# Optimization experiments

Hardware: AMD Instinct MI355X
Metric: run time of the kernel (lower is better)

The kernel has to match this reference:

```python
import jax, jax.numpy as jnp
import numpy as np

N_NODES = 100000
N_EDGES = 1600000


def _tconv(x, src, dst, Wq, bq, Wk, bk, Wv, bv, Ws, bs):
    """PyG TransformerConv (heads=1, concat=True, root_weight=True), eval mode."""
    n = x.shape[0]
    q = x @ Wq + bq          # [N, d]
    k = x @ Wk + bk
    v = x @ Wv + bv
    scale = 1.0 / jnp.sqrt(jnp.asarray(q.shape[1], q.dtype))
    # per-edge attention logits: query at destination, key at source
    alpha = jnp.sum(q[dst] * k[src], axis=-1) * scale       # [E]
    # segment softmax over incoming edges of each destination node
    m = jax.ops.segment_max(alpha, dst, num_segments=n)      # [N]
    e = jnp.exp(alpha - m[dst])
    s = jax.ops.segment_sum(e, dst, num_segments=n)          # [N]
    a = e / s[dst]                                           # [E]
    agg = jax.ops.segment_sum(a[:, None] * v[src], dst, num_segments=n)  # [N, d]
    return agg + x @ Ws + bs  # skip connection (root_weight=True)


def setup_inputs() -> dict:
    key = jax.random.key(0)
    ks = jax.random.split(key, 20)
    x = jax.random.normal(ks[0], (N_NODES, 2), dtype=jnp.float32)
    edge_index = jax.random.randint(ks[1], (2, N_EDGES), 0, N_NODES, dtype=jnp.int64)
    def lin(k, din, dout):
        k1, k2 = jax.random.split(k)
        lim = 1.0 / np.sqrt(din)
        W = jax.random.uniform(k1, (din, dout), jnp.float32, -lim, lim)
        b = jax.random.uniform(k2, (dout,), jnp.float32, -lim, lim)
        return W, b
    Wq1, bq1 = lin(ks[2], 2, 256)
    Wk1, bk1 = lin(ks[3], 2, 256)
    Wv1, bv1 = lin(ks[4], 2, 256)
    Ws1, bs1 = lin(ks[5], 2, 256)
    Wq2, bq2 = lin(ks[6], 256, 2)
    Wk2, bk2 = lin(ks[7], 256, 2)
    Wv2, bv2 = lin(ks[8], 256, 2)
    Ws2, bs2 = lin(ks[9], 256, 2)
    return dict(x=x, edge_index=edge_index,
                Wq1=Wq1, bq1=bq1, Wk1=Wk1, bk1=bk1, Wv1=Wv1, bv1=bv1, Ws1=Ws1, bs1=bs1,
                Wq2=Wq2, bq2=bq2, Wk2=Wk2, bk2=bk2, Wv2=Wv2, bv2=bv2, Ws2=Ws2, bs2=bs2)


def reference(x, edge_index,
              Wq1, bq1, Wk1, bk1, Wv1, bv1, Ws1, bs1,
              Wq2, bq2, Wk2, bk2, Wv2, bv2, Ws2, bs2):
    src, dst = edge_index[0], edge_index[1]
    h = _tconv(x, src, dst, Wq1, bq1, Wk1, bk1, Wv1, bv1, Ws1, bs1)
    h = jax.nn.relu(h)
    # F.dropout is identity in eval mode
    h = _tconv(h, src, dst, Wq2, bq2, Wk2, bk2, Wv2, bv2, Ws2, bs2)
    return jax.nn.log_softmax(h, axis=1)
```

## Files before the change

kernel.cpp:

```cpp
#include <hip/hip_runtime.h>


#define R_LOG2   8
#define R_DSTS   256
#define BE       4096
#define MAXNB    512
#define S_SLICES 8
#define RSQRT2   0.70710678118654752f

__device__ __forceinline__ int wave_excl_scan(int v, int lane, int& total) {
    int incl = v;
#pragma unroll
    for (int o = 1; o < 64; o <<= 1) {
        int t = __shfl_up(incl, o);
        if (lane >= o) incl += t;
    }
    total = __shfl(incl, 63);
    return incl - v;
}

__global__ void coeff_k(const float* __restrict__ Wq1, const float* __restrict__ bq1,
                        const float* __restrict__ Wk1, const float* __restrict__ bk1,
                        float* __restrict__ coeff) {
    __shared__ float part[4][9];
    int c = threadIdx.x;
    float wq0 = Wq1[c], wq1 = Wq1[256 + c];
    float wk0 = Wk1[c], wk1 = Wk1[256 + c];
    float bq = bq1[c], bk = bk1[c];
    float vals[9] = { wq0 * wk0, wq0 * wk1, wq1 * wk0, wq1 * wk1,
                      wq0 * bk,  wq1 * bk,  bq * wk0,  bq * wk1,  bq * bk };
    int lane = c & 63, w = c >> 6;
#pragma unroll
    for (int i = 0; i < 9; ++i) {
        float v = vals[i];
#pragma unroll
        for (int o = 32; o > 0; o >>= 1) v += __shfl_xor(v, o);
        if (lane == 0) part[w][i] = v;
    }
    __syncthreads();
    if (c < 9) coeff[c] = part[0][c] + part[1][c] + part[2][c] + part[3][c];
}

__global__ __launch_bounds__(256) void count_k(
        const int* __restrict__ dst, int* __restrict__ C,
        int NB, int NBlk, int E) {
    __shared__ int hist[MAXNB];
    int t = threadIdx.x;
    for (int i = t; i < NB; i += 256) hist[i] = 0;
    __syncthreads();
    int base = blockIdx.x * BE;
    int nloc = E - base; if (nloc > BE) nloc = BE;
    int nv = nloc >> 2;
    const int4* d4 = (const int4*)(dst + base);
    for (int i = t; i < nv; i += 256) {
        int4 v = d4[i];
        atomicAdd(&hist[v.x >> R_LOG2], 1);
        atomicAdd(&hist[v.y >> R_LOG2], 1);
        atomicAdd(&hist[v.z >> R_LOG2], 1);
        atomicAdd(&hist[v.w >> R_LOG2], 1);
    }
    for (int i = (nv << 2) + t; i < nloc; i += 256)
        atomicAdd(&hist[dst[base + i] >> R_LOG2], 1);
    __syncthreads();
    for (int b = t; b < NB; b += 256)
        C[(size_t)b * NBlk + blockIdx.x] = hist[b];
}

__global__ __launch_bounds__(256) void rowscan_k(
        int* __restrict__ C, int* __restrict__ rowTotal, int NB, int NBlk) {
    int lane = threadIdx.x & 63;
    int row = blockIdx.x * 4 + (threadIdx.x >> 6);
    if (row >= NB) return;
    int carry = 0;
    for (int j0 = 0; j0 < NBlk; j0 += 64) {
        int idx = j0 + lane;
        int v = (idx < NBlk) ? C[(size_t)row * NBlk + idx] : 0;
        int tot, ex = wave_excl_scan(v, lane, tot);
        if (idx < NBlk) C[(size_t)row * NBlk + idx] = ex + carry;
        carry += tot;
    }
    if (lane == 0) rowTotal[row] = carry;
}

__global__ __launch_bounds__(64) void bucketscan_k(
        const int* __restrict__ rowTotal, int* __restrict__ bucketBase, int NB) {
    int lane = threadIdx.x;
    int carry = 0;
    for (int j0 = 0; j0 < NB; j0 += 64) {
        int idx = j0 + lane;
        int v = (idx < NB) ? rowTotal[idx] : 0;
        int tot, ex = wave_excl_scan(v, lane, tot);
        if (idx < NB) bucketBase[idx] = ex + carry;
        carry += tot;
    }
    if (lane == 0) bucketBase[NB] = carry;
}

__global__ __launch_bounds__(256) void scatter2_k(
        const int* __restrict__ src, const int* __restrict__ dst,
        const int* __restrict__ C, const int* __restrict__ bucketBase,
        int* __restrict__ recs, int NB, int NBlk, int E) {
    __shared__ int hist[MAXNB];
    __shared__ int lofs[MAXNB];
    __shared__ int gbase[MAXNB];
    __shared__ int stage[BE];
    __shared__ unsigned short sbkt[BE];
    __shared__ int wsum[4];
    int t = threadIdx.x;
    for (int i = t; i < NB; i += 256) hist[i] = 0;
    __syncthreads();

    int blk = blockIdx.x;
    int base = blk * BE;
    int nloc = E - base; if (nloc > BE) nloc = BE;
    int nv = nloc >> 2;
    const int4* d4 = (const int4*)(dst + base);
    const int4* s4 = (const int4*)(src + base);

    for (int i = t; i < nv; i += 256) {
        int4 v = d4[i];
        atomicAdd(&hist[v.x >> R_LOG2], 1);
        atomicAdd(&hist[v.y >> R_LOG2], 1);
        atomicAdd(&hist[v.z >> R_LOG2], 1);
        atomicAdd(&hist[v.w >> R_LOG2], 1);
    }
    for (int i = (nv << 2) + t; i < nloc; i += 256)
        atomicAdd(&hist[dst[base + i] >> R_LOG2], 1);
    __syncthreads();

    {
        int i0 = 2 * t, i1 = 2 * t + 1;
        int a = (i0 < NB) ? hist[i0] : 0;
        int b = (i1 < NB) ? hist[i1] : 0;
        int s = a + b;
        int lane = t & 63, w = t >> 6;
        int incl = s;
#pragma unroll
        for (int o = 1; o < 64; o <<= 1) {
            int u = __shfl_up(incl, o);
            if (lane >= o) incl += u;
        }
        if (lane == 63) wsum[w] = incl;
        __syncthreads();
        int ex = incl - s;
        for (int j = 0; j < w; ++j) ex += wsum[j];
        if (i0 < NB) lofs[i0] = ex;
        if (i1 < NB) lofs[i1] = ex + a;
    }
    __syncthreads();

    for (int b = t; b < NB; b += 256) {
        gbase[b] = bucketBase[b] + C[(size_t)b * NBlk + blk] - lofs[b];
        hist[b] = 0;
    }
    __syncthreads();

    for (int i = t; i < nv; i += 256) {
        int4 dv = d4[i];
        int4 sv = s4[i];
        int d, b, r, p;
        d = dv.x; b = d >> R_LOG2; r = atomicAdd(&hist[b], 1); p = lofs[b] + r;
        stage[p] = sv.x | ((d & (R_DSTS - 1)) << 17); sbkt[p] = (unsigned short)b;
        d = dv.y; b = d >> R_LOG2; r = atomicAdd(&hist[b], 1); p = lofs[b] + r;
        stage[p] = sv.y | ((d & (R_DSTS - 1)) << 17); sbkt[p] = (unsigned short)b;
        d = dv.z; b = d >> R_LOG2; r = atomicAdd(&hist[b], 1); p = lofs[b] + r;
        stage[p] = sv.z | ((d & (R_DSTS - 1)) << 17); sbkt[p] = (unsigned short)b;
        d = dv.w; b = d >> R_LOG2; r = atomicAdd(&hist[b], 1); p = lofs[b] + r;
        stage[p] = sv.w | ((d & (R_DSTS - 1)) << 17); sbkt[p] = (unsigned short)b;
    }
    for (int i = (nv << 2) + t; i < nloc; i += 256) {
        int d = dst[base + i];
        int b = d >> R_LOG2;
        int r = atomicAdd(&hist[b], 1);
        int p = lofs[b] + r;
        stage[p] = src[base + i] | ((d & (R_DSTS - 1)) << 17);
        sbkt[p] = (unsigned short)b;
    }
    __syncthreads();

    for (int i = t; i < nloc; i += 256)
        recs[gbase[sbkt[i]] + i] = stage[i];
}

__global__ __launch_bounds__(256) void l1r_k(
        const float* __restrict__ x, const float* __restrict__ coeff,
        const int* __restrict__ recs, const int* __restrict__ bucketBase,
        float* __restrict__ part, int N) {
    __shared__ float p0[R_DSTS], p1[R_DSTS], pc[R_DSTS];
    __shared__ float ac[3 * R_DSTS];
    int t = threadIdx.x;
    int bs = blockIdx.x;
    int b = bs / S_SLICES;
    int sl = bs - b * S_SLICES;
    int nbase = b << R_LOG2;
    int rem = N - nbase; if (rem > R_DSTS) rem = R_DSTS;

    ac[t] = 0.f; ac[256 + t] = 0.f; ac[512 + t] = 0.f;
    if (t < rem) {
        float2 xd = ((const float2*)x)[nbase + t];
        float c0 = coeff[0], c1 = coeff[1], c2 = coeff[2], c3 = coeff[3];
        float c4 = coeff[4], c5 = coeff[5], c6 = coeff[6], c7 = coeff[7];
        float c8 = coeff[8];
        p0[t] = c0 * xd.x + c2 * xd.y + c6;
        p1[t] = c1 * xd.x + c3 * xd.y + c7;
        pc[t] = c4 * xd.x + c5 * xd.y + c8;
    }
    __syncthreads();

    int eb = bucketBase[b], ee = bucketBase[b + 1];
    int len = (ee - eb + S_SLICES - 1) / S_SLICES;
    int lo = eb + sl * len;
    int hi = lo + len; if (hi > ee) hi = ee;
    for (int i = lo + t; i < hi; i += 256) {
        int rec = recs[i];
        int s = rec & 0x1FFFF;
        int dl = (rec >> 17) & (R_DSTS - 1);
        float2 xs = ((const float2*)x)[s];
        float w = __expf((p0[dl] * xs.x + p1[dl] * xs.y + pc[dl]) * 0.0625f);
        atomicAdd(&ac[dl], w);
        atomicAdd(&ac[256 + dl], w * xs.x);
        atomicAdd(&ac[512 + dl], w * xs.y);
    }
    __syncthreads();

    float* dp = part + (size_t)bs * (3 * R_DSTS);
    dp[t] = ac[t];
    dp[256 + t] = ac[256 + t];
    dp[512 + t] = ac[512 + t];
}

__global__ __launch_bounds__(256) void node_k(
        const float* __restrict__ x, const float* __restrict__ part,
        const float* __restrict__ Wv1, const float* __restrict__ bv1,
        const float* __restrict__ Ws1, const float* __restrict__ bs1,
        const float* __restrict__ Wq2, const float* __restrict__ bq2,
        const float* __restrict__ Wk2, const float* __restrict__ bk2,
        const float* __restrict__ Wv2, const float* __restrict__ bv2,
        const float* __restrict__ Ws2, const float* __restrict__ bs2,
        float* __restrict__ q2, float4* __restrict__ kv2,
        float* __restrict__ hs2, int N) {
    int t = threadIdx.x;
    int b = blockIdx.x;
    int n = (b << R_LOG2) + t;
    if (n >= N) return;

    const float* pp = part + (size_t)b * S_SLICES * (3 * R_DSTS);
    float s = 0.f, sx0 = 0.f, sx1 = 0.f;
#pragma unroll
    for (int sl = 0; sl < S_SLICES; ++sl) {
        s   += pp[sl * 768 + t];
        sx0 += pp[sl * 768 + 256 + t];
        sx1 += pp[sl * 768 + 512 + t];
    }

    float a0 = 0.f, a1 = 0.f, he = 0.f;
    if (s > 0.f) {
        float inv = 1.0f / s;
        a0 = sx0 * inv; a1 = sx1 * inv; he = 1.f;
    }
    float2 xd = ((const float2*)x)[n];

    float acc0 = 0.f, acc1 = 0.f, acc2 = 0.f, acc3 = 0.f;
    float acc4 = 0.f, acc5 = 0.f, acc6 = 0.f, acc7 = 0.f;
#pragma unroll 8
    for (int c = 0; c < 256; ++c) {
        float h = a0 * Wv1[c] + a1 * Wv1[256 + c]
                + xd.x * Ws1[c] + xd.y * Ws1[256 + c]
                + he * bv1[c] + bs1[c];
        h = fmaxf(h, 0.f);
        acc0 += h * Wq2[2 * c];
        acc1 += h * Wq2[2 * c + 1];
        acc2 += h * Wk2[2 * c];
        acc3 += h * Wk2[2 * c + 1];
        acc4 += h * Wv2[2 * c];
        acc5 += h * Wv2[2 * c + 1];
        acc6 += h * Ws2[2 * c];
        acc7 += h * Ws2[2 * c + 1];
    }
    ((float2*)q2)[n]  = make_float2(acc0 + bq2[0], acc1 + bq2[1]);
    kv2[n] = make_float4(acc2 + bk2[0], acc3 + bk2[1],
                         acc4 + bv2[0], acc5 + bv2[1]);
    ((float2*)hs2)[n] = make_float2(acc6 + bs2[0], acc7 + bs2[1]);
}

__global__ __launch_bounds__(256) void l2r_k(
        const float* __restrict__ q2, const float4* __restrict__ kv2,
        const int* __restrict__ recs, const int* __restrict__ bucketBase,
        float* __restrict__ part, int N) {
    __shared__ float qx[R_DSTS], qy[R_DSTS];
    __shared__ float ac[3 * R_DSTS];
    int t = threadIdx.x;
    int bs = blockIdx.x;
    int b = bs / S_SLICES;
    int sl = bs - b * S_SLICES;
    int nbase = b << R_LOG2;
    int rem = N - nbase; if (rem > R_DSTS) rem = R_DSTS;

    ac[t] = 0.f; ac[256 + t] = 0.f; ac[512 + t] = 0.f;
    if (t < rem) {
        float2 q = ((const float2*)q2)[nbase + t];
        qx[t] = q.x * RSQRT2;
        qy[t] = q.y * RSQRT2;
    }
    __syncthreads();

    int eb = bucketBase[b], ee = bucketBase[b + 1];
    int len = (ee - eb + S_SLICES - 1) / S_SLICES;
    int lo = eb + sl * len;
    int hi = lo + len; if (hi > ee) hi = ee;
    for (int i = lo + t; i < hi; i += 256) {
        int rec = recs[i];
        int s = rec & 0x1FFFF;
        int dl = (rec >> 17) & (R_DSTS - 1);
        float4 kv = kv2[s];
        float w = __expf(qx[dl] * kv.x + qy[dl] * kv.y);
        atomicAdd(&ac[dl], w);
        atomicAdd(&ac[256 + dl], w * kv.z);
        atomicAdd(&ac[512 + dl], w * kv.w);
    }
    __syncthreads();

    float* dp = part + (size_t)bs * (3 * R_DSTS);
    dp[t] = ac[t];
    dp[256 + t] = ac[256 + t];
    dp[512 + t] = ac[512 + t];
}

__global__ __launch_bounds__(256) void out2_k(
        const float* __restrict__ part, const float* __restrict__ hs2,
        float* __restrict__ out, int N) {
    int t = threadIdx.x;
    int b = blockIdx.x;
    int n = (b << R_LOG2) + t;
    if (n >= N) return;

    const float* pp = part + (size_t)b * S_SLICES * (3 * R_DSTS);
    float s = 0.f, sv0 = 0.f, sv1 = 0.f;
#pragma unroll
    for (int sl = 0; sl < S_SLICES; ++sl) {
        s   += pp[sl * 768 + t];
        sv0 += pp[sl * 768 + 256 + t];
        sv1 += pp[sl * 768 + 512 + t];
    }
    float g0 = 0.f, g1 = 0.f;
    if (s > 0.f) {
        float inv = 1.0f / s;
        g0 = sv0 * inv; g1 = sv1 * inv;
    }
    float2 hs = ((const float2*)hs2)[n];
    float o0 = g0 + hs.x;
    float o1 = g1 + hs.y;
    float mx = fmaxf(o0, o1), mn = fminf(o0, o1);
    float lse = mx + log1pf(__expf(mn - mx));
    ((float2*)out)[n] = make_float2(o0 - lse, o1 - lse);
}

extern "C" void kernel_launch(void* const* d_in, const int* in_sizes, int n_in,
                              void* d_out, int out_size, void* d_ws, size_t ws_size,
                              hipStream_t stream) {
    const float* x   = (const float*)d_in[0];
    const int*   ei  = (const int*)d_in[1];
    const float* Wq1 = (const float*)d_in[2];
    const float* bq1 = (const float*)d_in[3];
    const float* Wk1 = (const float*)d_in[4];
    const float* bk1 = (const float*)d_in[5];
    const float* Wv1 = (const float*)d_in[6];
    const float* bv1 = (const float*)d_in[7];
    const float* Ws1 = (const float*)d_in[8];
    const float* bs1 = (const float*)d_in[9];
    const float* Wq2 = (const float*)d_in[10];
    const float* bq2 = (const float*)d_in[11];
    const float* Wk2 = (const float*)d_in[12];
    const float* bk2 = (const float*)d_in[13];
    const float* Wv2 = (const float*)d_in[14];
    const float* bv2 = (const float*)d_in[15];
    const float* Ws2 = (const float*)d_in[16];
    const float* bs2 = (const float*)d_in[17];

    const int N = in_sizes[0] / 2;
    const int E = in_sizes[1] / 2;
    const int* src = ei;
    const int* dst = ei + E;

    const int NB   = (N + R_DSTS - 1) >> R_LOG2;
    const int NBlk = (E + BE - 1) / BE;

    float* ws = (float*)d_ws;
    size_t off = 0;
    float* coeff      = ws + off;            off += 16;
    int*   bucketBase = (int*)(ws + off);    off += (size_t)NB + 1;
    int*   rowTotal   = (int*)(ws + off);    off += NB;
    int*   C          = (int*)(ws + off);    off += (size_t)NB * NBlk;
    int*   recs       = (int*)(ws + off);    off += E;
    off = (off + 3) & ~(size_t)3;
    float* part       = ws + off;            off += (size_t)NB * S_SLICES * 3 * R_DSTS;
    float4* kv2       = (float4*)(ws + off); off += 4 * (size_t)N;
    float* q2         = ws + off;            off += 2 * (size_t)N;
    float* hs2        = ws + off;            off += 2 * (size_t)N;

    coeff_k<<<1, 256, 0, stream>>>(Wq1, bq1, Wk1, bk1, coeff);
    count_k<<<NBlk, 256, 0, stream>>>(dst, C, NB, NBlk, E);
    rowscan_k<<<(NB + 3) / 4, 256, 0, stream>>>(C, rowTotal, NB, NBlk);
    bucketscan_k<<<1, 64, 0, stream>>>(rowTotal, bucketBase, NB);
    scatter2_k<<<NBlk, 256, 0, stream>>>(src, dst, C, bucketBase, recs, NB, NBlk, E);
    l1r_k<<<NB * S_SLICES, 256, 0, stream>>>(x, coeff, recs, bucketBase, part, N);
    node_k<<<NB, 256, 0, stream>>>(x, part, Wv1, bv1, Ws1, bs1,
                                   Wq2, bq2, Wk2, bk2, Wv2, bv2, Ws2, bs2,
                                   q2, kv2, hs2, N);
    l2r_k<<<NB * S_SLICES, 256, 0, stream>>>(q2, kv2, recs, bucketBase, part, N);
    out2_k<<<NB, 256, 0, stream>>>(part, hs2, (float*)d_out, N);
}
```

Before: 135.2 us.

## Split per-node projection across 8 lanes with shared-memory weights

The node projection kernel now assigns 8 threads per node instead of one. Each thread reads one slice's partial sums, combines them with xor shuffles, and handles a strided quarter-chunk of the 256 hidden channels, reading weights staged once per block in shared memory as float4. The output kernel uses the same 8-lanes-per-node reduction over slices. The goal is more parallelism (8x more blocks) and cheaper weight reads, replacing the serial 256-iteration loop of global weight loads. The cost is shuffle reductions, each block staging the weights into shared memory, and only one of every eight lanes writing results.

Result: faster. 125.0 us (-7.6%).

```diff
diff --git a/kernel.cpp b/kernel.cpp
--- a/kernel.cpp
+++ b/kernel.cpp
@@ -229,7 +229,7 @@
     dp[512 + t] = ac[512 + t];
 }
 
-__global__ __launch_bounds__(256) void node_k(
+__global__ __launch_bounds__(256) void proj_k(
         const float* __restrict__ x, const float* __restrict__ part,
         const float* __restrict__ Wv1, const float* __restrict__ bv1,
         const float* __restrict__ Ws1, const float* __restrict__ bs1,
@@ -239,20 +239,37 @@
         const float* __restrict__ Ws2, const float* __restrict__ bs2,
         float* __restrict__ q2, float4* __restrict__ kv2,
         float* __restrict__ hs2, int N) {
-    int t = threadIdx.x;
-    int b = blockIdx.x;
-    int n = (b << R_LOG2) + t;
+    __shared__ float sW[14][256];
+    int t = threadIdx.x;
+    sW[0][t]  = Wv1[t];
+    sW[1][t]  = Wv1[256 + t];
+    sW[2][t]  = Ws1[t];
+    sW[3][t]  = Ws1[256 + t];
+    sW[4][t]  = bv1[t];
+    sW[5][t]  = bs1[t];
+    sW[6][t]  = Wq2[2 * t];
+    sW[7][t]  = Wq2[2 * t + 1];
+    sW[8][t]  = Wk2[2 * t];
+    sW[9][t]  = Wk2[2 * t + 1];
+    sW[10][t] = Wv2[2 * t];
+    sW[11][t] = Wv2[2 * t + 1];
+    sW[12][t] = Ws2[2 * t];
+    sW[13][t] = Ws2[2 * t + 1];
+    __syncthreads();
+
+    int g = t & 7;
+    int n = blockIdx.x * 32 + (t >> 3);
     if (n >= N) return;
-
-    const float* pp = part + (size_t)b * S_SLICES * (3 * R_DSTS);
-    float s = 0.f, sx0 = 0.f, sx1 = 0.f;
-#pragma unroll
-    for (int sl = 0; sl < S_SLICES; ++sl) {
-        s   += pp[sl * 768 + t];
-        sx0 += pp[sl * 768 + 256 + t];
-        sx1 += pp[sl * 768 + 512 + t];
-    }
-
+    int b = n >> R_LOG2, idx = n & (R_DSTS - 1);
+
+    const float* pp = part + ((size_t)(b * S_SLICES + g)) * (3 * R_DSTS) + idx;
+    float s = pp[0], sx0 = pp[256], sx1 = pp[512];
+#pragma unroll
+    for (int m = 1; m < 8; m <<= 1) {
+        s   += __shfl_xor(s, m);
+        sx0 += __shfl_xor(sx0, m);
+        sx1 += __shfl_xor(sx1, m);
+    }
     float a0 = 0.f, a1 = 0.f, he = 0.f;
     if (s > 0.f) {
         float inv = 1.0f / s;
@@ -262,25 +279,47 @@
 
     float acc0 = 0.f, acc1 = 0.f, acc2 = 0.f, acc3 = 0.f;
     float acc4 = 0.f, acc5 = 0.f, acc6 = 0.f, acc7 = 0.f;
-#pragma unroll 8
-    for (int c = 0; c < 256; ++c) {
-        float h = a0 * Wv1[c] + a1 * Wv1[256 + c]
-                + xd.x * Ws1[c] + xd.y * Ws1[256 + c]
-                + he * bv1[c] + bs1[c];
-        h = fmaxf(h, 0.f);
-        acc0 += h * Wq2[2 * c];
-        acc1 += h * Wq2[2 * c + 1];
-        acc2 += h * Wk2[2 * c];
-        acc3 += h * Wk2[2 * c + 1];
-        acc4 += h * Wv2[2 * c];
-        acc5 += h * Wv2[2 * c + 1];
-        acc6 += h * Ws2[2 * c];
-        acc7 += h * Ws2[2 * c + 1];
-    }
-    ((float2*)q2)[n]  = make_float2(acc0 + bq2[0], acc1 + bq2[1]);
-    kv2[n] = make_float4(acc2 + bk2[0], acc3 + bk2[1],
-                         acc4 + bv2[0], acc5 + bv2[1]);
-    ((float2*)hs2)[n] = make_float2(acc6 + bs2[0], acc7 + bs2[1]);
+#pragma unroll
+    for (int j = 0; j < 8; ++j) {
+        int ci = g + 8 * j;
+        float4 w0 = ((const float4*)sW[0])[ci];
+        float4 w1 = ((const float4*)sW[1])[ci];
+        float4 w2 = ((const float4*)sW[2])[ci];
+        float4 w3 = ((const float4*)sW[3])[ci];
+        float4 w4 = ((const float4*)sW[4])[ci];
+        float4 w5 = ((const float4*)sW[5])[ci];
+        float4 h;
+        h.x = fmaxf(a0 * w0.x + a1 * w1.x + xd.x * w2.x + xd.y * w3.x + he * w4.x + w5.x, 0.f);
+        h.y = fmaxf(a0 * w0.y + a1 * w1.y + xd.x * w2.y + xd.y * w3.y + he * w4.y + w5.y, 0.f);
+        h.z = fmaxf(a0 * w0.z + a1 * w1.z + xd.x * w2.z + xd.y * w3.z + he * w4.z + w5.z, 0.f);
+        h.w = fmaxf(a0 * w0.w + a1 * w1.w + xd.x * w2.w + xd.y * w3.w + he * w4.w + w5.w, 0.f);
+        float4 u;
+        u = ((const float4*)sW[6])[ci];  acc0 += h.x*u.x + h.y*u.y + h.z*u.z + h.w*u.w;
+        u = ((const float4*)sW[7])[ci];  acc1 += h.x*u.x + h.y*u.y + h.z*u.z + h.w*u.w;
+        u = ((const float4*)sW[8])[ci];  acc2 += h.x*u.x + h.y*u.y + h.z*u.z + h.w*u.w;
+        u = ((const float4*)sW[9])[ci];  acc3 += h.x*u.x + h.y*u.y + h.z*u.z + h.w*u.w;
+        u = ((const float4*)sW[10])[ci]; acc4 += h.x*u.x + h.y*u.y + h.z*u.z + h.w*u.w;
+        u = ((const float4*)sW[11])[ci]; acc5 += h.x*u.x + h.y*u.y + h.z*u.z + h.w*u.w;
+        u = ((const float4*)sW[12])[ci]; acc6 += h.x*u.x + h.y*u.y + h.z*u.z + h.w*u.w;
+        u = ((const float4*)sW[13])[ci]; acc7 += h.x*u.x + h.y*u.y + h.z*u.z + h.w*u.w;
+    }
+#pragma unroll
+    for (int m = 1; m < 8; m <<= 1) {
+        acc0 += __shfl_xor(acc0, m);
+        acc1 += __shfl_xor(acc1, m);
+        acc2 += __shfl_xor(acc2, m);
+        acc3 += __shfl_xor(acc3, m);
+        acc4 += __shfl_xor(acc4, m);
+        acc5 += __shfl_xor(acc5, m);
+        acc6 += __shfl_xor(acc6, m);
+        acc7 += __shfl_xor(acc7, m);
+    }
+    if (g == 0) {
+        ((float2*)q2)[n]  = make_float2(acc0 + bq2[0], acc1 + bq2[1]);
+        kv2[n] = make_float4(acc2 + bk2[0], acc3 + bk2[1],
+                             acc4 + bv2[0], acc5 + bv2[1]);
+        ((float2*)hs2)[n] = make_float2(acc6 + bs2[0], acc7 + bs2[1]);
+    }
 }
 
 __global__ __launch_bounds__(256) void l2r_k(
@@ -326,22 +365,25 @@
     dp[512 + t] = ac[512 + t];
 }
 
-__global__ __launch_bounds__(256) void out2_k(
+__global__ __launch_bounds__(256) void out2x_k(
         const float* __restrict__ part, const float* __restrict__ hs2,
         float* __restrict__ out, int N) {
     int t = threadIdx.x;
-    int b = blockIdx.x;
-    int n = (b << R_LOG2) + t;
+    int g = t & 7;
+    int n = blockIdx.x * 32 + (t >> 3);
     if (n >= N) return;
-
-    const float* pp = part + (size_t)b * S_SLICES * (3 * R_DSTS);
-    float s = 0.f, sv0 = 0.f, sv1 = 0.f;
-#pragma unroll
-    for (int sl = 0; sl < S_SLICES; ++sl) {
-        s   += pp[sl * 768 + t];
-        sv0 += pp[sl * 768 + 256 + t];
-        sv1 += pp[sl * 768 + 512 + t];
-    }
+    int b = n >> R_LOG2, idx = n & (R_DSTS - 1);
+
+    const float* pp = part + ((size_t)(b * S_SLICES + g)) * (3 * R_DSTS) + idx;
+    float s = pp[0], sv0 = pp[256], sv1 = pp[512];
+#pragma unroll
+    for (int m = 1; m < 8; m <<= 1) {
+        s   += __shfl_xor(s, m);
+        sv0 += __shfl_xor(sv0, m);
+        sv1 += __shfl_xor(sv1, m);
+    }
+    if (g != 0) return;
+
     float g0 = 0.f, g1 = 0.f;
     if (s > 0.f) {
         float inv = 1.0f / s;
@@ -398,15 +440,17 @@
     float* q2         = ws + off;            off += 2 * (size_t)N;
     float* hs2        = ws + off;            off += 2 * (size_t)N;
 
+    const int gP = (N + 31) / 32;
+
     coeff_k<<<1, 256, 0, stream>>>(Wq1, bq1, Wk1, bk1, coeff);
     count_k<<<NBlk, 256, 0, stream>>>(dst, C, NB, NBlk, E);
     rowscan_k<<<(NB + 3) / 4, 256, 0, stream>>>(C, rowTotal, NB, NBlk);
     bucketscan_k<<<1, 64, 0, stream>>>(rowTotal, bucketBase, NB);
     scatter2_k<<<NBlk, 256, 0, stream>>>(src, dst, C, bucketBase, recs, NB, NBlk, E);
     l1r_k<<<NB * S_SLICES, 256, 0, stream>>>(x, coeff, recs, bucketBase, part, N);
-    node_k<<<NB, 256, 0, stream>>>(x, part, Wv1, bv1, Ws1, bs1,
+    proj_k<<<gP, 256, 0, stream>>>(x, part, Wv1, bv1, Ws1, bs1,
                                    Wq2, bq2, Wk2, bk2, Wv2, bv2, Ws2, bs2,
                                    q2, kv2, hs2, N);
     l2r_k<<<NB * S_SLICES, 256, 0, stream>>>(q2, kv2, recs, bucketBase, part, N);
-    out2_k<<<NB, 256, 0, stream>>>(part, hs2, (float*)d_out, N);
-}
+    out2x_k<<<gP, 256, 0, stream>>>(part, hs2, (float*)d_out, N);
+}
```
